# Performance work log

Measured on AMD Instinct MI355X. Metric: run time of the kernel, lower is better.

The kernel has to match this reference:

```python
import jax, jax.numpy as jnp
import numpy as np

N, E, F_IN, R, B = 50000, 800000, 128, 8, 64
H1, H2, EMB, OUT = 64, 128, 16, 32
BN_EPS = 1e-5


def _rgcn(x, src, dst, et, W, root, b, num_nodes, num_rel):
    # per-relation transform of all nodes: [R, N, out]
    h = jnp.einsum('nd,rde->rne', x, W)
    msg = h[et, src]                      # [E, out] gather per edge
    seg = dst * num_rel + et              # composite (dst, relation) key
    cnt = jax.ops.segment_sum(jnp.ones((src.shape[0],), x.dtype), seg,
                              num_segments=num_nodes * num_rel)
    norm = (1.0 / jnp.maximum(cnt, 1.0))[seg]   # mean aggr per (dst, rel)
    agg = jax.ops.segment_sum(msg * norm[:, None], dst, num_segments=num_nodes)
    return agg + x @ root + b


def _linear(x, w, b):
    return x @ w + b


def setup_inputs() -> dict:
    key = jax.random.key(0)
    ks = jax.random.split(key, 24)
    s = lambda d: 1.0 / np.sqrt(d)
    inp = {
        'x': jax.random.normal(ks[0], (N, F_IN), jnp.float32),
        'edge_index': jax.random.randint(ks[1], (2, E), 0, N, jnp.int32),
        'edge_type': jax.random.randint(ks[2], (E,), 0, R, jnp.int32),
        'batch': jnp.sort(jax.random.randint(ks[3], (N,), 0, B, jnp.int32)),
        # RGCNConv 1: F_IN -> H1
        'W1': jax.random.normal(ks[4], (R, F_IN, H1), jnp.float32) * s(F_IN),
        'root1': jax.random.normal(ks[5], (F_IN, H1), jnp.float32) * s(F_IN),
        'b1': jnp.zeros((H1,), jnp.float32),
        # RGCNConv 2: H1 -> H2
        'W2': jax.random.normal(ks[6], (R, H1, H2), jnp.float32) * s(H1),
        'root2': jax.random.normal(ks[7], (H1, H2), jnp.float32) * s(H1),
        'b2': jnp.zeros((H2,), jnp.float32),
        # fc_emb: Linear(128,64) -> BN(64) -> LeakyReLU(0.2) -> Linear(64,16)
        'fc1_w': jax.random.normal(ks[8], (H2, H1), jnp.float32) * s(H2),
        'fc1_b': jnp.zeros((H1,), jnp.float32),
        'bn_g': jnp.ones((H1,), jnp.float32),
        'bn_b': jnp.zeros((H1,), jnp.float32),
        'fc2_w': jax.random.normal(ks[9], (H1, EMB), jnp.float32) * s(H1),
        'fc2_b': jnp.zeros((EMB,), jnp.float32),
        # decoder: Linear(16,64) -> LeakyReLU(0.2) -> Linear(64,OUT)
        'dec1_w': jax.random.normal(ks[10], (EMB, H1), jnp.float32) * s(EMB),
        'dec1_b': jnp.zeros((H1,), jnp.float32),
        'dec2_w': jax.random.normal(ks[11], (H1, OUT), jnp.float32) * s(H1),
        'dec2_b': jnp.zeros((OUT,), jnp.float32),
    }
    return inp


def reference(x, edge_index, edge_type, batch, W1, root1, b1, W2, root2, b2,
              fc1_w, fc1_b, bn_g, bn_b, fc2_w, fc2_b,
              dec1_w, dec1_b, dec2_w, dec2_b):
    src, dst = edge_index[0], edge_index[1]
    h = jax.nn.relu(_rgcn(x, src, dst, edge_type, W1, root1, b1, N, R))
    # dropout is identity in eval mode
    h = jax.nn.relu(_rgcn(h, src, dst, edge_type, W2, root2, b2, N, R))
    # dual pooling per graph
    cnt = jax.ops.segment_sum(jnp.ones((N,), h.dtype), batch, num_segments=B)
    mean_p = jax.ops.segment_sum(h, batch, num_segments=B) / jnp.maximum(cnt, 1.0)[:, None]
    max_p = jax.ops.segment_max(h, batch, num_segments=B)
    g = mean_p + max_p                                    # [B, 128]
    # fc_emb (BatchNorm with batch statistics, biased var, eps=1e-5)
    z = _linear(g, fc1_w, fc1_b)
    mu = jnp.mean(z, axis=0)
    var = jnp.mean((z - mu) ** 2, axis=0)
    z = (z - mu) / jnp.sqrt(var + BN_EPS) * bn_g + bn_b
    z = jax.nn.leaky_relu(z, 0.2)
    emb = _linear(z, fc2_w, fc2_b)                        # [B, 16]
    # decoder
    d = jax.nn.leaky_relu(_linear(emb, dec1_w, dec1_b), 0.2)
    pred = _linear(d, dec2_w, dec2_b)                     # [B, OUT]
    return (pred, emb)
```

## Files before the change

### kernel.cpp

```cpp
#include <hip/hip_runtime.h>

#define NNODES 50000
#define NEDGES 800000
#define FIN    128
#define NREL   8
#define NB     64
#define H1D    64
#define H2D    128
#define BN_EPS 1e-5f

__global__ __launch_bounds__(256) void count_edges_kernel(
    const int* __restrict__ dst, const int* __restrict__ et,
    int* __restrict__ cnt_dr, int* __restrict__ cnt_d, int E)
{
    int e = blockIdx.x * 256 + threadIdx.x;
    if (e < E) {
        int t = dst[e];
        atomicAdd(&cnt_dr[t * NREL + et[e]], 1);
        atomicAdd(&cnt_d[t], 1);
    }
}

__global__ __launch_bounds__(256) void inv_kernel(int* __restrict__ cnt_i,
                                                  float* __restrict__ invf, int n)
{
    int i = blockIdx.x * 256 + threadIdx.x;
    if (i < n) {
        int c = cnt_i[i];
        invf[i] = 1.0f / (float)(c > 1 ? c : 1);
    }
}

__global__ __launch_bounds__(1024) void scan_kernel(
    const int* __restrict__ cnt_d, int* __restrict__ off_d, int* __restrict__ cur_d)
{
    __shared__ int part[1024];
    const int T = 1024;
    const int C = (NNODES + T - 1) / T;
    int t = threadIdx.x;
    int base = t * C;
    int s = 0;
    for (int i = 0; i < C; ++i) {
        int idx = base + i;
        if (idx < NNODES) s += cnt_d[idx];
    }
    part[t] = s;
    __syncthreads();
    for (int d = 1; d < T; d <<= 1) {
        int v = (t >= d) ? part[t - d] : 0;
        __syncthreads();
        part[t] += v;
        __syncthreads();
    }
    int run = (t == 0) ? 0 : part[t - 1];
    for (int i = 0; i < C; ++i) {
        int idx = base + i;
        if (idx < NNODES) {
            off_d[idx] = run;
            cur_d[idx] = run;
            run += cnt_d[idx];
        }
    }
    if (t == T - 1) off_d[NNODES] = run;
}

__global__ __launch_bounds__(256) void scatter_kernel(
    const int* __restrict__ src, const int* __restrict__ dst,
    const int* __restrict__ et, int* __restrict__ cur_d,
    int* __restrict__ sorted_pk, int E)
{
    int e = blockIdx.x * 256 + threadIdx.x;
    if (e < E) {
        int pos = atomicAdd(&cur_d[dst[e]], 1);
        sorted_pk[pos] = src[e] * NREL + et[e];
    }
}

#define G1_NBX 25
__global__ __launch_bounds__(256) void gemm1_kernel(
    const float* __restrict__ X, const float* __restrict__ W1,
    const float* __restrict__ root1, const float* __restrict__ bias1,
    float* __restrict__ h1t, float* __restrict__ agg1, int Nn)
{
    __shared__ float As[2][16][260];
    __shared__ float Bs[2][16][64];
    const int id  = blockIdx.x;
    const int xcd = id & 7;
    const int j   = id >> 3;
    const int r   = j / G1_NBX;
    const int bx  = xcd * G1_NBX + (j % G1_NBX);
    const int m0  = bx * 256;
    if (m0 >= Nn) return;
    const float* Bsrc = (r < 8) ? (W1 + (size_t)r * FIN * H1D) : root1;

    const int tid = threadIdx.x;
    const int ty = tid >> 3, tx = tid & 7;
    const int ak = tid & 15, am = tid >> 4;
    const int bn = tid & 63, bk = tid >> 6;

    float ar[16], br[4];
#pragma unroll
    for (int i = 0; i < 16; ++i) {
        int row = m0 + am + i * 16;
        ar[i] = (row < Nn) ? X[(size_t)row * FIN + ak] : 0.f;
    }
#pragma unroll
    for (int i = 0; i < 4; ++i) br[i] = Bsrc[(size_t)(bk + i * 4) * 64 + bn];
#pragma unroll
    for (int i = 0; i < 16; ++i) As[0][ak][am + i * 16] = ar[i];
#pragma unroll
    for (int i = 0; i < 4; ++i) Bs[0][bk + i * 4][bn] = br[i];
    __syncthreads();

    float acc[8][8] = {};
    const int NCH = FIN / 16;
    for (int c = 0; c < NCH; ++c) {
        const int cur = c & 1;
        if (c + 1 < NCH) {
            const int kc = (c + 1) * 16;
#pragma unroll
            for (int i = 0; i < 16; ++i) {
                int row = m0 + am + i * 16;
                ar[i] = (row < Nn) ? X[(size_t)row * FIN + kc + ak] : 0.f;
            }
#pragma unroll
            for (int i = 0; i < 4; ++i)
                br[i] = Bsrc[(size_t)(kc + bk + i * 4) * 64 + bn];
        }
#pragma unroll
        for (int k = 0; k < 16; ++k) {
            const float4 a0 = *reinterpret_cast<const float4*>(&As[cur][k][ty * 4]);
            const float4 a1 = *reinterpret_cast<const float4*>(&As[cur][k][ty * 4 + 128]);
            const float4 b0 = *reinterpret_cast<const float4*>(&Bs[cur][k][tx * 4]);
            const float4 b1v = *reinterpret_cast<const float4*>(&Bs[cur][k][tx * 4 + 32]);
            const float a[8] = {a0.x, a0.y, a0.z, a0.w, a1.x, a1.y, a1.z, a1.w};
            const float b[8] = {b0.x, b0.y, b0.z, b0.w, b1v.x, b1v.y, b1v.z, b1v.w};
#pragma unroll
            for (int i = 0; i < 8; ++i)
#pragma unroll
                for (int jj = 0; jj < 8; ++jj) acc[i][jj] += a[i] * b[jj];
        }
        if (c + 1 < NCH) {
            const int nxt = cur ^ 1;
#pragma unroll
            for (int i = 0; i < 16; ++i) As[nxt][ak][am + i * 16] = ar[i];
#pragma unroll
            for (int i = 0; i < 4; ++i) Bs[nxt][bk + i * 4][bn] = br[i];
        }
        __syncthreads();
    }

#pragma unroll
    for (int i = 0; i < 8; ++i) {
        int row = m0 + ty * 4 + (i & 3) + (i >> 2) * 128;
        if (row >= Nn) continue;
        int col = tx * 4;
        if (r < 8) {
            float4 v0 = make_float4(acc[i][0], acc[i][1], acc[i][2], acc[i][3]);
            float4 v1 = make_float4(acc[i][4], acc[i][5], acc[i][6], acc[i][7]);
            *reinterpret_cast<float4*>(&h1t[(size_t)row * 512 + r * 64 + col]) = v0;
            *reinterpret_cast<float4*>(&h1t[(size_t)row * 512 + r * 64 + col + 32]) = v1;
        } else {
            float4 v0 = make_float4(acc[i][0] + bias1[col], acc[i][1] + bias1[col + 1],
                                    acc[i][2] + bias1[col + 2], acc[i][3] + bias1[col + 3]);
            float4 v1 = make_float4(acc[i][4] + bias1[col + 32], acc[i][5] + bias1[col + 33],
                                    acc[i][6] + bias1[col + 34], acc[i][7] + bias1[col + 35]);
            *reinterpret_cast<float4*>(&agg1[(size_t)row * H1D + col]) = v0;
            *reinterpret_cast<float4*>(&agg1[(size_t)row * H1D + col + 32]) = v1;
        }
    }
}

__global__ __launch_bounds__(256) void agg1_gather_kernel(
    const int* __restrict__ sorted_pk, const int* __restrict__ off_d,
    const float* __restrict__ inv, const float* __restrict__ h1t,
    float* __restrict__ agg1)
{
    int d = blockIdx.x * 4 + (threadIdx.x >> 6);
    int lane = threadIdx.x & 63;
    if (d >= NNODES) return;
    int beg = off_d[d], end = off_d[d + 1];
    float acc = agg1[(size_t)d * H1D + lane];
    for (int i = beg; i < end; ++i) {
        int k = sorted_pk[i];
        float w = inv[d * NREL + (k & 7)];
        acc += h1t[(size_t)k * 64 + lane] * w;
    }
    agg1[(size_t)d * H1D + lane] = acc;
}

__global__ __launch_bounds__(256) void agg2_gather_kernel(
    const int* __restrict__ sorted_pk, const int* __restrict__ off_d,
    const float* __restrict__ inv, const float* __restrict__ agg1,
    float* __restrict__ aggin2)
{
    int d = blockIdx.x * 4 + (threadIdx.x >> 6);
    int lane = threadIdx.x & 63;
    if (d >= NNODES) return;
    int beg = off_d[d], end = off_d[d + 1];
    float acc[NREL] = {};
    for (int i = beg; i < end; ++i) {
        int k = sorted_pk[i];
        int s = k >> 3, r = k & 7;
        float v = fmaxf(agg1[(size_t)s * H1D + lane], 0.f) * inv[d * NREL + r];
#pragma unroll
        for (int rr = 0; rr < NREL; ++rr) acc[rr] += (r == rr) ? v : 0.f;
    }
    float* row = &aggin2[(size_t)d * 512 + lane];
#pragma unroll
    for (int rr = 0; rr < NREL; ++rr) row[rr * 64] = acc[rr];
}

__global__ __launch_bounds__(256) void gemm2_kernel(
    const float* __restrict__ aggin2, const float* __restrict__ agg1,
    const float* __restrict__ W2, const float* __restrict__ root2,
    const float* __restrict__ b2, float* __restrict__ agg2, int Nn)
{
    __shared__ float As[2][16][68];
    __shared__ float Bs[2][16][128];
    const int m0 = blockIdx.x * 64;
    if (m0 >= Nn) return;
    const int tid = threadIdx.x;
    const int ty = tid >> 4, tx = tid & 15;
    const int ak = tid & 15, am = tid >> 4;
    const int bn = tid & 127, bk = tid >> 7;

    float ar[4], br[8];
#pragma unroll
    for (int i = 0; i < 4; ++i) {
        int row = m0 + am + i * 16;
        ar[i] = (row < Nn) ? aggin2[(size_t)row * 512 + ak] : 0.f;
    }
#pragma unroll
    for (int i = 0; i < 8; ++i) br[i] = W2[(size_t)(bk + i * 2) * H2D + bn];
#pragma unroll
    for (int i = 0; i < 4; ++i) As[0][ak][am + i * 16] = ar[i];
#pragma unroll
    for (int i = 0; i < 8; ++i) Bs[0][bk + i * 2][bn] = br[i];
    __syncthreads();

    float acc[4][8] = {};
    const int NCH = 576 / 16;
    for (int c = 0; c < NCH; ++c) {
        const int cur = c & 1;
        if (c + 1 < NCH) {
            const int kc = (c + 1) * 16;
            if (kc < 512) {
#pragma unroll
                for (int i = 0; i < 4; ++i) {
                    int row = m0 + am + i * 16;
                    ar[i] = (row < Nn) ? aggin2[(size_t)row * 512 + kc + ak] : 0.f;
                }
#pragma unroll
                for (int i = 0; i < 8; ++i)
                    br[i] = W2[(size_t)(kc + bk + i * 2) * H2D + bn];
            } else {
#pragma unroll
                for (int i = 0; i < 4; ++i) {
                    int row = m0 + am + i * 16;
                    ar[i] = (row < Nn)
                          ? fmaxf(agg1[(size_t)row * H1D + (kc - 512) + ak], 0.f) : 0.f;
                }
#pragma unroll
                for (int i = 0; i < 8; ++i)
                    br[i] = root2[(size_t)(kc - 512 + bk + i * 2) * H2D + bn];
            }
        }
#pragma unroll
        for (int k = 0; k < 16; ++k) {
            const float4 a0 = *reinterpret_cast<const float4*>(&As[cur][k][ty * 4]);
            const float4 b0 = *reinterpret_cast<const float4*>(&Bs[cur][k][tx * 4]);
            const float4 b1v = *reinterpret_cast<const float4*>(&Bs[cur][k][tx * 4 + 64]);
            const float a[4] = {a0.x, a0.y, a0.z, a0.w};
            const float b[8] = {b0.x, b0.y, b0.z, b0.w, b1v.x, b1v.y, b1v.z, b1v.w};
#pragma unroll
            for (int i = 0; i < 4; ++i)
#pragma unroll
                for (int jj = 0; jj < 8; ++jj) acc[i][jj] += a[i] * b[jj];
        }
        if (c + 1 < NCH) {
            const int nxt = cur ^ 1;
#pragma unroll
            for (int i = 0; i < 4; ++i) As[nxt][ak][am + i * 16] = ar[i];
#pragma unroll
            for (int i = 0; i < 8; ++i) Bs[nxt][bk + i * 2][bn] = br[i];
        }
        __syncthreads();
    }

#pragma unroll
    for (int i = 0; i < 4; ++i) {
        int row = m0 + ty * 4 + i;
        if (row >= Nn) continue;
        int col = tx * 4;
        float4 v0 = make_float4(acc[i][0] + b2[col], acc[i][1] + b2[col + 1],
                                acc[i][2] + b2[col + 2], acc[i][3] + b2[col + 3]);
        float4 v1 = make_float4(acc[i][4] + b2[col + 64], acc[i][5] + b2[col + 65],
                                acc[i][6] + b2[col + 66], acc[i][7] + b2[col + 67]);
        *reinterpret_cast<float4*>(&agg2[(size_t)row * H2D + col]) = v0;
        *reinterpret_cast<float4*>(&agg2[(size_t)row * H2D + col + 64]) = v1;
    }
}

__global__ __launch_bounds__(64) void batchseg_kernel(const int* __restrict__ batch,
                                                      float* __restrict__ cntb, int Nn)
{
    __shared__ int lo_s[NB];
    int b = threadIdx.x;
    int lo = 0, hi = Nn;
    while (lo < hi) { int mid = (lo + hi) >> 1; if (batch[mid] < b) lo = mid + 1; else hi = mid; }
    lo_s[b] = lo;
    __syncthreads();
    int end = (b == NB - 1) ? Nn : lo_s[b + 1];
    cntb[b] = (float)(end - lo_s[b]);
}

__global__ __launch_bounds__(256) void pool_kernel(
    const float* __restrict__ agg2, const int* __restrict__ batch,
    float* __restrict__ psum, float* __restrict__ pmax, int Nn)
{
    int c = threadIdx.x & 127;
    int p = threadIdx.x >> 7;
    int n0 = blockIdx.x * 128;
    int nend = n0 + 128 < Nn ? n0 + 128 : Nn;
    float sum = 0.f, mx = 0.f;
    int cur = -1;
    for (int n = n0 + p; n < nend; n += 2) {
        int b = batch[n];
        float v = fmaxf(agg2[(size_t)n * H2D + c], 0.f);
        if (b != cur) {
            if (cur >= 0) {
                atomicAdd(&psum[cur * H2D + c], sum);
                atomicMax((int*)&pmax[cur * H2D + c], __float_as_int(mx));
            }
            cur = b; sum = 0.f; mx = 0.f;
        }
        sum += v; mx = fmaxf(mx, v);
    }
    if (cur >= 0) {
        atomicAdd(&psum[cur * H2D + c], sum);
        atomicMax((int*)&pmax[cur * H2D + c], __float_as_int(mx));
    }
}

__global__ __launch_bounds__(256) void head_kernel(
    const float* __restrict__ psum, const float* __restrict__ pmax,
    const float* __restrict__ cntb,
    const float* __restrict__ fc1_w, const float* __restrict__ fc1_b,
    const float* __restrict__ bn_g, const float* __restrict__ bn_b,
    const float* __restrict__ fc2_w, const float* __restrict__ fc2_b,
    const float* __restrict__ dec1_w, const float* __restrict__ dec1_b,
    const float* __restrict__ dec2_w, const float* __restrict__ dec2_b,
    float* __restrict__ out)
{
    __shared__ float gs[64 * 128];
    __shared__ float zs[64 * 64];
    __shared__ float mu[64], var_[64];
    float* es = gs;
    float* ds = gs + 1024;
    const int t = threadIdx.x;

    for (int i = t; i < 64 * 128; i += 256) {
        int b = i >> 7;
        gs[i] = psum[i] / fmaxf(cntb[b], 1.f) + pmax[i];
    }
    __syncthreads();
    for (int o = t; o < 4096; o += 256) {
        int r = o >> 6, cc = o & 63;
        float a = fc1_b[cc];
        for (int k = 0; k < 128; ++k) a += gs[r * 128 + k] * fc1_w[k * 64 + cc];
        zs[o] = a;
    }
    __syncthreads();
    if (t < 64) {
        float s = 0.f;
        for (int r = 0; r < 64; ++r) s += zs[r * 64 + t];
        float m = s * (1.f / 64.f);
        float v = 0.f;
        for (int r = 0; r < 64; ++r) { float d = zs[r * 64 + t] - m; v += d * d; }
        mu[t] = m; var_[t] = v * (1.f / 64.f);
    }
    __syncthreads();
    for (int o = t; o < 4096; o += 256) {
        int cc = o & 63;
        float z = (zs[o] - mu[cc]) / sqrtf(var_[cc] + BN_EPS) * bn_g[cc] + bn_b[cc];
        zs[o] = (z > 0.f) ? z : 0.2f * z;
    }
    __syncthreads();
    for (int o = t; o < 1024; o += 256) {
        int r = o >> 4, cc = o & 15;
        float a = fc2_b[cc];
        for (int k = 0; k < 64; ++k) a += zs[r * 64 + k] * fc2_w[k * 16 + cc];
        es[o] = a;
        out[2048 + o] = a;
    }
    __syncthreads();
    for (int o = t; o < 4096; o += 256) {
        int r = o >> 6, cc = o & 63;
        float a = dec1_b[cc];
        for (int k = 0; k < 16; ++k) a += es[r * 16 + k] * dec1_w[k * 64 + cc];
        ds[o] = (a > 0.f) ? a : 0.2f * a;
    }
    __syncthreads();
    for (int o = t; o < 2048; o += 256) {
        int r = o >> 5, cc = o & 31;
        float a = dec2_b[cc];
        for (int k = 0; k < 64; ++k) a += ds[r * 64 + k] * dec2_w[k * 32 + cc];
        out[o] = a;
    }
}

extern "C" void kernel_launch(void* const* d_in, const int* in_sizes, int n_in,
                              void* d_out, int out_size, void* d_ws, size_t ws_size,
                              hipStream_t stream)
{
    const float* x      = (const float*)d_in[0];
    const int*   eidx   = (const int*)d_in[1];
    const int*   etype  = (const int*)d_in[2];
    const int*   batch  = (const int*)d_in[3];
    const float* W1     = (const float*)d_in[4];
    const float* root1  = (const float*)d_in[5];
    const float* b1     = (const float*)d_in[6];
    const float* W2     = (const float*)d_in[7];
    const float* root2  = (const float*)d_in[8];
    const float* b2     = (const float*)d_in[9];
    const float* fc1_w  = (const float*)d_in[10];
    const float* fc1_b  = (const float*)d_in[11];
    const float* bn_g   = (const float*)d_in[12];
    const float* bn_b   = (const float*)d_in[13];
    const float* fc2_w  = (const float*)d_in[14];
    const float* fc2_b  = (const float*)d_in[15];
    const float* dec1_w = (const float*)d_in[16];
    const float* dec1_b = (const float*)d_in[17];
    const float* dec2_w = (const float*)d_in[18];
    const float* dec2_b = (const float*)d_in[19];
    float* out = (float*)d_out;

    const int* src = eidx;
    const int* dst = eidx + NEDGES;

    float* ws     = (float*)d_ws;
    float* h1t    = ws;
    float* agg1   = h1t  + (size_t)NNODES * 512;
    float* agg2   = agg1 + (size_t)NNODES * H1D;
    float* inv    = agg2 + (size_t)NNODES * H2D;
    float* psum   = inv  + (size_t)NNODES * NREL;
    float* pmax   = psum + NB * H2D;
    float* cntb   = pmax + NB * H2D;

    int* cnt_d     = (int*)agg2;
    int* off_d     = cnt_d + NNODES;
    int* cur_d     = off_d + NNODES + 1;
    int* sorted_pk = cur_d + NNODES;

    hipMemsetAsync(inv, 0, (size_t)NNODES * NREL * sizeof(int), stream);
    hipMemsetAsync(cnt_d, 0, NNODES * sizeof(int), stream);
    hipMemsetAsync(psum, 0, (2 * NB * H2D) * sizeof(float), stream);

    count_edges_kernel<<<(NEDGES + 255) / 256, 256, 0, stream>>>(dst, etype, (int*)inv, cnt_d, NEDGES);
    inv_kernel<<<(NNODES * NREL + 255) / 256, 256, 0, stream>>>((int*)inv, inv, NNODES * NREL);
    scan_kernel<<<1, 1024, 0, stream>>>(cnt_d, off_d, cur_d);
    scatter_kernel<<<(NEDGES + 255) / 256, 256, 0, stream>>>(src, dst, etype, cur_d, sorted_pk, NEDGES);

    gemm1_kernel<<<8 * G1_NBX * 9, 256, 0, stream>>>(x, W1, root1, b1, h1t, agg1, NNODES);

    agg1_gather_kernel<<<(NNODES + 3) / 4, 256, 0, stream>>>(sorted_pk, off_d, inv, h1t, agg1);

    float* aggin2 = h1t;
    agg2_gather_kernel<<<(NNODES + 3) / 4, 256, 0, stream>>>(sorted_pk, off_d, inv, agg1, aggin2);

    gemm2_kernel<<<(NNODES + 63) / 64, 256, 0, stream>>>(aggin2, agg1, W2, root2, b2, agg2, NNODES);

    batchseg_kernel<<<1, 64, 0, stream>>>(batch, cntb, NNODES);
    pool_kernel<<<(NNODES + 127) / 128, 256, 0, stream>>>(agg2, batch, psum, pmax, NNODES);

    head_kernel<<<1, 256, 0, stream>>>(psum, pmax, cntb, fc1_w, fc1_b, bn_g, bn_b,
                                       fc2_w, fc2_b, dec1_w, dec1_b, dec2_w, dec2_b, out);
}
```

Measured before the change: 882.0 us.

## Fuse graph pooling into gemm2 epilogue and use nontemporal stores for h1t

The relu, mean-sum and max pooling are moved into the gemm2 epilogue, so the separate pool kernel and the agg2 round trip through global memory go away. When a 64-row tile belongs to one graph, the block reduces in shared memory and issues one atomic per column; mixed tiles fall back to per-thread atomics. gemm1 writes h1t with nontemporal stores to reduce cache pollution. The shared-memory reduction adds extra syncs to the gemm2 tail.

```diff
diff --git a/kernel.cpp b/kernel.cpp
--- a/kernel.cpp
+++ b/kernel.cpp
@@ -8,6 +8,8 @@
 #define H1D    64
 #define H2D    128
 #define BN_EPS 1e-5f
+
+typedef float floatx4 __attribute__((ext_vector_type(4)));
 
 __global__ __launch_bounds__(256) void count_edges_kernel(
     const int* __restrict__ dst, const int* __restrict__ et,
@@ -156,10 +158,12 @@
         if (row >= Nn) continue;
         int col = tx * 4;
         if (r < 8) {
-            float4 v0 = make_float4(acc[i][0], acc[i][1], acc[i][2], acc[i][3]);
-            float4 v1 = make_float4(acc[i][4], acc[i][5], acc[i][6], acc[i][7]);
-            *reinterpret_cast<float4*>(&h1t[(size_t)row * 512 + r * 64 + col]) = v0;
-            *reinterpret_cast<float4*>(&h1t[(size_t)row * 512 + r * 64 + col + 32]) = v1;
+            floatx4 v0 = {acc[i][0], acc[i][1], acc[i][2], acc[i][3]};
+            floatx4 v1 = {acc[i][4], acc[i][5], acc[i][6], acc[i][7]};
+            __builtin_nontemporal_store(v0,
+                reinterpret_cast<floatx4*>(&h1t[(size_t)row * 512 + r * 64 + col]));
+            __builtin_nontemporal_store(v1,
+                reinterpret_cast<floatx4*>(&h1t[(size_t)row * 512 + r * 64 + col + 32]));
         } else {
             float4 v0 = make_float4(acc[i][0] + bias1[col], acc[i][1] + bias1[col + 1],
                                     acc[i][2] + bias1[col + 2], acc[i][3] + bias1[col + 3]);
@@ -214,7 +218,8 @@
 __global__ __launch_bounds__(256) void gemm2_kernel(
     const float* __restrict__ aggin2, const float* __restrict__ agg1,
     const float* __restrict__ W2, const float* __restrict__ root2,
-    const float* __restrict__ b2, float* __restrict__ agg2, int Nn)
+    const float* __restrict__ b2, const int* __restrict__ batch,
+    float* __restrict__ psum, float* __restrict__ pmax, int Nn)
 {
     __shared__ float As[2][16][68];
     __shared__ float Bs[2][16][128];
@@ -288,17 +293,82 @@
         __syncthreads();
     }
 
-#pragma unroll
-    for (int i = 0; i < 4; ++i) {
-        int row = m0 + ty * 4 + i;
-        if (row >= Nn) continue;
-        int col = tx * 4;
-        float4 v0 = make_float4(acc[i][0] + b2[col], acc[i][1] + b2[col + 1],
-                                acc[i][2] + b2[col + 2], acc[i][3] + b2[col + 3]);
-        float4 v1 = make_float4(acc[i][4] + b2[col + 64], acc[i][5] + b2[col + 65],
-                                acc[i][6] + b2[col + 66], acc[i][7] + b2[col + 67]);
-        *reinterpret_cast<float4*>(&agg2[(size_t)row * H2D + col]) = v0;
-        *reinterpret_cast<float4*>(&agg2[(size_t)row * H2D + col + 64]) = v1;
+    float s[8], mxv[8];
+#pragma unroll
+    for (int j = 0; j < 8; ++j) { s[j] = 0.f; mxv[j] = 0.f; }
+
+    const int rowEnd = m0 + 63;
+    const bool fastpath = (rowEnd < Nn) && (batch[m0] == batch[rowEnd]);
+
+    if (fastpath) {
+        const int b = batch[m0];
+#pragma unroll
+        for (int i = 0; i < 4; ++i)
+#pragma unroll
+            for (int j = 0; j < 8; ++j) {
+                int col = tx * 4 + (j & 3) + (j >> 2) * 64;
+                float v = fmaxf(acc[i][j] + b2[col], 0.f);
+                s[j] += v; mxv[j] = fmaxf(mxv[j], v);
+            }
+        float* red = (float*)As;
+#pragma unroll
+        for (int j = 0; j < 8; ++j) {
+            int col = tx * 4 + (j & 3) + (j >> 2) * 64;
+            red[ty * 128 + col] = s[j];
+        }
+        __syncthreads();
+        if (tid < 128) {
+            float a = 0.f;
+            for (int t = 0; t < 16; ++t) a += red[t * 128 + tid];
+            atomicAdd(&psum[b * H2D + tid], a);
+        }
+        __syncthreads();
+#pragma unroll
+        for (int j = 0; j < 8; ++j) {
+            int col = tx * 4 + (j & 3) + (j >> 2) * 64;
+            red[ty * 128 + col] = mxv[j];
+        }
+        __syncthreads();
+        if (tid < 128) {
+            float a = 0.f;
+            for (int t = 0; t < 16; ++t) a = fmaxf(a, red[t * 128 + tid]);
+            atomicMax((int*)&pmax[b * H2D + tid], __float_as_int(a));
+        }
+    } else {
+        int bprev = -1;
+#pragma unroll
+        for (int i = 0; i < 4; ++i) {
+            int row = m0 + ty * 4 + i;
+            if (row >= Nn) break;
+            int b = batch[row];
+            if (b != bprev) {
+                if (bprev >= 0) {
+#pragma unroll
+                    for (int j = 0; j < 8; ++j) {
+                        int col = tx * 4 + (j & 3) + (j >> 2) * 64;
+                        atomicAdd(&psum[bprev * H2D + col], s[j]);
+                        atomicMax((int*)&pmax[bprev * H2D + col], __float_as_int(mxv[j]));
+                    }
+                }
+                bprev = b;
+#pragma unroll
+                for (int j = 0; j < 8; ++j) { s[j] = 0.f; mxv[j] = 0.f; }
+            }
+#pragma unroll
+            for (int j = 0; j < 8; ++j) {
+                int col = tx * 4 + (j & 3) + (j >> 2) * 64;
+                float v = fmaxf(acc[i][j] + b2[col], 0.f);
+                s[j] += v; mxv[j] = fmaxf(mxv[j], v);
+            }
+        }
+        if (bprev >= 0) {
+#pragma unroll
+            for (int j = 0; j < 8; ++j) {
+                int col = tx * 4 + (j & 3) + (j >> 2) * 64;
+                atomicAdd(&psum[bprev * H2D + col], s[j]);
+                atomicMax((int*)&pmax[bprev * H2D + col], __float_as_int(mxv[j]));
+            }
+        }
     }
 }
 
@@ -313,34 +383,6 @@
     __syncthreads();
     int end = (b == NB - 1) ? Nn : lo_s[b + 1];
     cntb[b] = (float)(end - lo_s[b]);
-}
-
-__global__ __launch_bounds__(256) void pool_kernel(
-    const float* __restrict__ agg2, const int* __restrict__ batch,
-    float* __restrict__ psum, float* __restrict__ pmax, int Nn)
-{
-    int c = threadIdx.x & 127;
-    int p = threadIdx.x >> 7;
-    int n0 = blockIdx.x * 128;
-    int nend = n0 + 128 < Nn ? n0 + 128 : Nn;
-    float sum = 0.f, mx = 0.f;
-    int cur = -1;
-    for (int n = n0 + p; n < nend; n += 2) {
-        int b = batch[n];
-        float v = fmaxf(agg2[(size_t)n * H2D + c], 0.f);
-        if (b != cur) {
-            if (cur >= 0) {
-                atomicAdd(&psum[cur * H2D + c], sum);
-                atomicMax((int*)&pmax[cur * H2D + c], __float_as_int(mx));
-            }
-            cur = b; sum = 0.f; mx = 0.f;
-        }
-        sum += v; mx = fmaxf(mx, v);
-    }
-    if (cur >= 0) {
-        atomicAdd(&psum[cur * H2D + c], sum);
-        atomicMax((int*)&pmax[cur * H2D + c], __float_as_int(mx));
-    }
 }
 
 __global__ __launch_bounds__(256) void head_kernel(
@@ -453,9 +495,9 @@
     int* cur_d     = off_d + NNODES + 1;
     int* sorted_pk = cur_d + NNODES;
 
-    hipMemsetAsync(inv, 0, (size_t)NNODES * NREL * sizeof(int), stream);
-    hipMemsetAsync(cnt_d, 0, NNODES * sizeof(int), stream);
-    hipMemsetAsync(psum, 0, (2 * NB * H2D) * sizeof(float), stream);
+    (void)hipMemsetAsync(inv, 0, (size_t)NNODES * NREL * sizeof(int), stream);
+    (void)hipMemsetAsync(cnt_d, 0, NNODES * sizeof(int), stream);
+    (void)hipMemsetAsync(psum, 0, (2 * NB * H2D) * sizeof(float), stream);
 
     count_edges_kernel<<<(NEDGES + 255) / 256, 256, 0, stream>>>(dst, etype, (int*)inv, cnt_d, NEDGES);
     inv_kernel<<<(NNODES * NREL + 255) / 256, 256, 0, stream>>>((int*)inv, inv, NNODES * NREL);
@@ -469,10 +511,10 @@
     float* aggin2 = h1t;
     agg2_gather_kernel<<<(NNODES + 3) / 4, 256, 0, stream>>>(sorted_pk, off_d, inv, agg1, aggin2);
 
-    gemm2_kernel<<<(NNODES + 63) / 64, 256, 0, stream>>>(aggin2, agg1, W2, root2, b2, agg2, NNODES);
-
     batchseg_kernel<<<1, 64, 0, stream>>>(batch, cntb, NNODES);
-    pool_kernel<<<(NNODES + 127) / 128, 256, 0, stream>>>(agg2, batch, psum, pmax, NNODES);
+
+    gemm2_kernel<<<(NNODES + 63) / 64, 256, 0, stream>>>(aggin2, agg1, W2, root2, b2,
+                                                         batch, psum, pmax, NNODES);
 
     head_kernel<<<1, 256, 0, stream>>>(psum, pmax, cntb, fc1_w, fc1_b, bn_g, bn_b,
                                        fc2_w, fc2_b, dec1_w, dec1_b, dec2_w, dec2_b, out);
```

Result: slower. 981.1 us (+11.2%).
